# Kernel optimization log

Hardware: AMD Instinct MI355X
Metric: run time of the kernel (lower is better)

## Reference

```python
import jax, jax.numpy as jnp
import numpy as np

B, S, D = 4, 2048, 1024
KEY_DIM, VALUE_DIM = 1024, 1024
BETA = 1.0 / np.sqrt(D)  # beta defaults to 1/sqrt(input dim), per build()


def setup_inputs() -> dict:
    key = jax.random.key(0)
    ks = jax.random.split(key, 9)
    inv = 1.0 / np.sqrt(D)
    return {
        "query": jax.random.normal(ks[0], (B, S, D), dtype=jnp.float32),
        "key": jax.random.normal(ks[1], (B, S, D), dtype=jnp.float32),
        "value": jax.random.normal(ks[2], (B, S, D), dtype=jnp.float32),
        "Wq": jax.random.normal(ks[3], (D, KEY_DIM), dtype=jnp.float32) * inv,
        "bq": jnp.zeros((KEY_DIM,), dtype=jnp.float32),
        "Wk": jax.random.normal(ks[4], (D, KEY_DIM), dtype=jnp.float32) * inv,
        "bk": jnp.zeros((KEY_DIM,), dtype=jnp.float32),
        "Wv": jax.random.normal(ks[5], (D, VALUE_DIM), dtype=jnp.float32) * inv,
        "bv": jnp.zeros((VALUE_DIM,), dtype=jnp.float32),
    }


def reference(query, key, value, Wq, bq, Wk, bk, Wv, bv):
    # Dense projections
    q = query @ Wq + bq          # [B, S, key_dim]
    k = key @ Wk + bk            # [B, S, key_dim]
    v = value @ Wv + bv          # [B, S, value_dim]
    # Scaled dot-product attention (beta applied AFTER matmul, as in source)
    scores = jnp.einsum("bik,bjk->bij", q, k)  # [B, S, S]
    A = jax.nn.softmax(BETA * scores, axis=-1)
    return jnp.einsum("bij,bjk->bik", A, v)    # [B, S, value_dim]
```

## Files before the change

### kernel.cpp

```cpp
#include <hip/hip_runtime.h>


typedef __bf16 bf16x8 __attribute__((ext_vector_type(8)));
typedef float f32x4 __attribute__((ext_vector_type(4)));

#define MIB ((size_t)1 << 20)

__device__ __forceinline__ unsigned short f2b(float f) {
  unsigned int u = __float_as_uint(f);
  return (unsigned short)((u + 0x7FFFu + ((u >> 16) & 1u)) >> 16);
}

__device__ __forceinline__ void async16(const void* g, void* l) {
  __builtin_amdgcn_global_load_lds(
      (const __attribute__((address_space(1))) unsigned int*)g,
      (__attribute__((address_space(3))) unsigned int*)l, 16, 0, 0);
}

template <int TN>
__device__ __forceinline__ void gemm_loop(
    const unsigned short* __restrict__ A, const unsigned short* __restrict__ Bt,
    unsigned short* lds_a, unsigned short* lds_b, int K, int m0, int n0,
    f32x4 (&acc)[4][TN / 32]) {
  constexpr int NI = TN / 32;
  const int tid = threadIdx.x;
  const int lane = tid & 63;
  const int wave = tid >> 6;
  const int wm = (wave >> 1) * 64;
  const int wn = (wave & 1) * (TN / 2);
  const int fr = lane & 15;
  const int q = lane >> 4;

  for (int kb = 0; kb < K; kb += 64) {
#pragma unroll
    for (int i = 0; i < 4; ++i) {
      const int e = i * 256 + tid;
      const int r = e >> 3;
      const int cg = (e & 7) ^ (r & 7);
      async16(A + (size_t)(m0 + r) * K + kb + cg * 8, &lds_a[e * 8]);
    }
#pragma unroll
    for (int i = 0; i < TN / 32; ++i) {
      const int e = i * 256 + tid;
      const int r = e >> 3;
      const int cg = (e & 7) ^ (r & 7);
      async16(Bt + (size_t)(n0 + r) * K + kb + cg * 8, &lds_b[e * 8]);
    }
    __syncthreads();

#pragma unroll
    for (int ks = 0; ks < 64; ks += 32) {
      const int kc = (ks >> 3) + q;
      bf16x8 av[4], bv[NI];
#pragma unroll
      for (int mi = 0; mi < 4; ++mi) {
        const int R = wm + mi * 16 + fr;
        av[mi] = *(const bf16x8*)&lds_a[R * 64 + ((kc ^ (R & 7)) << 3)];
      }
#pragma unroll
      for (int ni = 0; ni < NI; ++ni) {
        const int R = wn + ni * 16 + fr;
        bv[ni] = *(const bf16x8*)&lds_b[R * 64 + ((kc ^ (R & 7)) << 3)];
      }
#pragma unroll
      for (int mi = 0; mi < 4; ++mi)
#pragma unroll
        for (int ni = 0; ni < NI; ++ni)
          acc[mi][ni] = __builtin_amdgcn_mfma_f32_16x16x32_bf16(
              av[mi], bv[ni], acc[mi][ni], 0, 0, 0);
    }
    __syncthreads();
  }
}

struct ProjArgs {
  const unsigned short* A[3];
  const unsigned short* Bt[3];
  unsigned short* C[3];
  const float* bias[3];
};

__global__ __launch_bounds__(256) void proj_gemm(ProjArgs p) {
  __shared__ __align__(16) unsigned short lds_a[128 * 64];
  __shared__ __align__(16) unsigned short lds_b[64 * 64];

  const int z = blockIdx.z;
  const int m0 = blockIdx.y * 128;
  const int n0 = blockIdx.x * 64;

  f32x4 acc[4][2] = {};
  gemm_loop<64>(p.A[z], p.Bt[z], lds_a, lds_b, 1024, m0, n0, acc);

  const int lane = threadIdx.x & 63;
  const int wave = threadIdx.x >> 6;
  const int wm = (wave >> 1) * 64;
  const int wn = (wave & 1) * 32;
  const int fr = lane & 15;
  const float* bias = p.bias[z];

  if (z != 2) {
    unsigned short* C = p.C[z];
#pragma unroll
    for (int mi = 0; mi < 4; ++mi) {
#pragma unroll
      for (int ni = 0; ni < 2; ++ni) {
        const int col = n0 + wn + ni * 16 + fr;
        const float bb = bias[col];
        const int rowb = m0 + wm + mi * 16 + (lane >> 4) * 4;
#pragma unroll
        for (int r = 0; r < 4; ++r)
          C[(size_t)(rowb + r) * 1024 + col] = f2b(acc[mi][ni][r] + bb);
      }
    }
  } else {
    unsigned short* C = p.C[2] + (size_t)(m0 >> 11) * (2048 * 1024);
#pragma unroll
    for (int mi = 0; mi < 4; ++mi) {
#pragma unroll
      for (int ni = 0; ni < 2; ++ni) {
        const int col = n0 + wn + ni * 16 + fr;
        const float bb = bias[col];
        const int rowb = (m0 + wm + mi * 16 + (lane >> 4) * 4) & 2047;
        ushort4 o = make_ushort4(f2b(acc[mi][ni][0] + bb), f2b(acc[mi][ni][1] + bb),
                                 f2b(acc[mi][ni][2] + bb), f2b(acc[mi][ni][3] + bb));
        *(ushort4*)&C[(size_t)col * 2048 + rowb] = o;
      }
    }
  }
}

template <int TN>
__global__ __launch_bounds__(256) void gemm_f32(
    const unsigned short* __restrict__ A, const unsigned short* __restrict__ Bt,
    float* __restrict__ C, int K, int ldc, long long sA, long long sB,
    long long sC) {
  __shared__ __align__(16) unsigned short lds_a[128 * 64];
  __shared__ __align__(16) unsigned short lds_b[TN * 64];
  const int bz = blockIdx.z;
  A += (long long)bz * sA;
  Bt += (long long)bz * sB;
  C += (long long)bz * sC;
  const int m0 = blockIdx.y * 128;
  const int n0 = blockIdx.x * TN;

  f32x4 acc[4][TN / 32] = {};
  gemm_loop<TN>(A, Bt, lds_a, lds_b, K, m0, n0, acc);

  const int lane = threadIdx.x & 63;
  const int wave = threadIdx.x >> 6;
  const int wm = (wave >> 1) * 64;
  const int wn = (wave & 1) * (TN / 2);
  const int fr = lane & 15;
#pragma unroll
  for (int mi = 0; mi < 4; ++mi) {
#pragma unroll
    for (int ni = 0; ni < TN / 32; ++ni) {
      const int col = n0 + wn + ni * 16 + fr;
      const int rowb = m0 + wm + mi * 16 + (lane >> 4) * 4;
#pragma unroll
      for (int r = 0; r < 4; ++r)
        C[(size_t)(rowb + r) * ldc + col] = acc[mi][ni][r];
    }
  }
}

__global__ __launch_bounds__(256) void cast3(
    const float4* __restrict__ a, const float4* __restrict__ b,
    const float4* __restrict__ c, ushort4* __restrict__ oa,
    ushort4* __restrict__ ob, ushort4* __restrict__ oc, int n4) {
  const int i = blockIdx.x * 256 + threadIdx.x;
  if (i >= n4) return;
  const float4* src = (blockIdx.y == 0) ? a : (blockIdx.y == 1) ? b : c;
  ushort4* dst = (blockIdx.y == 0) ? oa : (blockIdx.y == 1) ? ob : oc;
  float4 v = src[i];
  dst[i] = make_ushort4(f2b(v.x), f2b(v.y), f2b(v.z), f2b(v.w));
}

__global__ __launch_bounds__(256) void transpose3(
    const float* __restrict__ w0, const float* __restrict__ w1,
    const float* __restrict__ w2, unsigned short* __restrict__ t0,
    unsigned short* __restrict__ t1, unsigned short* __restrict__ t2) {
  __shared__ float t[32][33];
  const int K = 1024, N = 1024;
  const float* W = (blockIdx.z == 0) ? w0 : (blockIdx.z == 1) ? w1 : w2;
  unsigned short* WT = (blockIdx.z == 0) ? t0 : (blockIdx.z == 1) ? t1 : t2;
  const int n0 = blockIdx.x * 32, k0 = blockIdx.y * 32;
  const int tx = threadIdx.x, ty = threadIdx.y;
#pragma unroll
  for (int i = 0; i < 32; i += 8)
    t[ty + i][tx] = W[(size_t)(k0 + ty + i) * N + (n0 + tx)];
  __syncthreads();
#pragma unroll
  for (int i = 0; i < 32; i += 8)
    WT[(size_t)(n0 + ty + i) * K + (k0 + tx)] = f2b(t[tx][ty + i]);
}

__global__ __launch_bounds__(256) void softmax_rows(const float* __restrict__ S,
                                                    unsigned short* __restrict__ P) {
  const int cols = 2048;
  const size_t row = blockIdx.x;
  const float4* srow = (const float4*)(S + row * cols);
  const int tid = threadIdx.x;
  const int lane = tid & 63;
  const int wave = tid >> 6;

  float4 a = srow[tid];
  float4 b = srow[tid + 256];

  float mx = fmaxf(fmaxf(fmaxf(a.x, a.y), fmaxf(a.z, a.w)),
                   fmaxf(fmaxf(b.x, b.y), fmaxf(b.z, b.w)));
#pragma unroll
  for (int o = 1; o < 64; o <<= 1) mx = fmaxf(mx, __shfl_xor(mx, o));

  __shared__ float red[8];
  if (lane == 0) red[wave] = mx;
  __syncthreads();
  mx = fmaxf(fmaxf(red[0], red[1]), fmaxf(red[2], red[3]));

  const float c = 0.03125f * 1.4426950408889634f;
  float4 pa, pb;
  pa.x = exp2f((a.x - mx) * c); pa.y = exp2f((a.y - mx) * c);
  pa.z = exp2f((a.z - mx) * c); pa.w = exp2f((a.w - mx) * c);
  pb.x = exp2f((b.x - mx) * c); pb.y = exp2f((b.y - mx) * c);
  pb.z = exp2f((b.z - mx) * c); pb.w = exp2f((b.w - mx) * c);

  float sum = pa.x + pa.y + pa.z + pa.w + pb.x + pb.y + pb.z + pb.w;
#pragma unroll
  for (int o = 1; o < 64; o <<= 1) sum += __shfl_xor(sum, o);
  if (lane == 0) red[4 + wave] = sum;
  __syncthreads();
  sum = red[4] + red[5] + red[6] + red[7];

  const float inv = 1.0f / sum;
  ushort4* prow = (ushort4*)(P + row * cols);
  prow[tid] = make_ushort4(f2b(pa.x * inv), f2b(pa.y * inv), f2b(pa.z * inv),
                           f2b(pa.w * inv));
  prow[tid + 256] = make_ushort4(f2b(pb.x * inv), f2b(pb.y * inv),
                                 f2b(pb.z * inv), f2b(pb.w * inv));
}

extern "C" void kernel_launch(void* const* d_in, const int* in_sizes, int n_in,
                              void* d_out, int out_size, void* d_ws, size_t ws_size,
                              hipStream_t stream) {
  const float* query = (const float*)d_in[0];
  const float* key_ = (const float*)d_in[1];
  const float* value = (const float*)d_in[2];
  const float* Wq = (const float*)d_in[3];
  const float* bq = (const float*)d_in[4];
  const float* Wk = (const float*)d_in[5];
  const float* bk = (const float*)d_in[6];
  const float* Wv = (const float*)d_in[7];
  const float* bv = (const float*)d_in[8];
  float* out = (float*)d_out;

  char* ws = (char*)d_ws;
  unsigned short* WqT = (unsigned short*)ws;
  unsigned short* WkT = WqT + (size_t)1024 * 1024;
  unsigned short* WvT = WkT + (size_t)1024 * 1024;
  unsigned short* Xq = (unsigned short*)(ws + 6 * MIB);
  unsigned short* Xk = Xq + (size_t)8192 * 1024;
  unsigned short* Xv = Xk + (size_t)8192 * 1024;
  unsigned short* qb = (unsigned short*)(ws + 54 * MIB);
  unsigned short* kb = (unsigned short*)(ws + 70 * MIB);
  unsigned short* vT = (unsigned short*)(ws + 86 * MIB);
  float* sc = (float*)(ws + 102 * MIB);
  unsigned short* P = (unsigned short*)(ws + 6 * MIB);

  const int n4 = (4 * 2048 * 1024) / 4;
  cast3<<<dim3(n4 / 256, 3), 256, 0, stream>>>(
      (const float4*)query, (const float4*)key_, (const float4*)value,
      (ushort4*)Xq, (ushort4*)Xk, (ushort4*)Xv, n4);

  transpose3<<<dim3(32, 32, 3), dim3(32, 8), 0, stream>>>(Wq, Wk, Wv, WqT, WkT,
                                                          WvT);

  ProjArgs pa;
  pa.A[0] = Xq;  pa.A[1] = Xk;  pa.A[2] = Xv;
  pa.Bt[0] = WqT; pa.Bt[1] = WkT; pa.Bt[2] = WvT;
  pa.C[0] = qb;  pa.C[1] = kb;  pa.C[2] = vT;
  pa.bias[0] = bq; pa.bias[1] = bk; pa.bias[2] = bv;
  proj_gemm<<<dim3(16, 64, 3), 256, 0, stream>>>(pa);

  gemm_f32<64><<<dim3(32, 16, 4), 256, 0, stream>>>(
      qb, kb, sc, 1024, 2048, 2048LL * 1024, 2048LL * 1024, 2048LL * 2048);

  softmax_rows<<<8192, 256, 0, stream>>>(sc, P);

  gemm_f32<64><<<dim3(16, 16, 4), 256, 0, stream>>>(
      P, vT, out, 2048, 1024, 2048LL * 2048, 1024LL * 2048, 2048LL * 1024);
}
```

Before: 339.3 us.

## Replace GEMMs with 256x256 double-buffered 8-wave pipelined kernel and split-K PV

Replaces the 128x64 single-buffered GEMM loop with a 256x256 tile, 512-thread core that double-buffers LDS in half-tiles. It interleaves async global->LDS staging with MFMA quadrants, using raw barriers, explicit waitcnts and setprio. Projection and score GEMMs use this core. The PV GEMM is split in two along K for occupancy, writing two partial outputs that an extra add kernel sums. This raises data reuse and overlaps memory with compute, at the cost of 128KB LDS per block and an extra float buffer pass for the split-K reduction.

```diff
diff --git a/kernel.cpp b/kernel.cpp
--- a/kernel.cpp
+++ b/kernel.cpp
@@ -17,59 +17,164 @@
       (__attribute__((address_space(3))) unsigned int*)l, 16, 0, 0);
 }
 
-template <int TN>
-__device__ __forceinline__ void gemm_loop(
+__device__ __forceinline__ void barrier_raw() {
+  asm volatile("" ::: "memory");
+  __builtin_amdgcn_s_barrier();
+  asm volatile("" ::: "memory");
+}
+
+__device__ __forceinline__ void stage_half(
+    const unsigned short* __restrict__ src, unsigned short* dst, int ld,
+    int tid) {
+#pragma unroll
+  for (int i = 0; i < 2; ++i) {
+    const int e = i * 512 + tid;
+    const int r = e >> 3;
+    const int cg = (e & 7) ^ (r & 7);
+    async16(src + (size_t)r * ld + cg * 8, dst + e * 8);
+  }
+}
+
+template <int MO, int NO>
+__device__ __forceinline__ void quad16(f32x4 (&acc)[8][4],
+                                       const bf16x8 (&AV)[4][2],
+                                       const bf16x8 (&BV)[2][2]) {
+#pragma unroll
+  for (int mi = 0; mi < 4; ++mi)
+#pragma unroll
+    for (int ni = 0; ni < 2; ++ni)
+#pragma unroll
+      for (int ks = 0; ks < 2; ++ks)
+        acc[MO + mi][NO + ni] = __builtin_amdgcn_mfma_f32_16x16x32_bf16(
+            AV[mi][ks], BV[ni][ks], acc[MO + mi][NO + ni], 0, 0, 0);
+}
+
+__device__ __forceinline__ void gemm256_core(
     const unsigned short* __restrict__ A, const unsigned short* __restrict__ Bt,
-    unsigned short* lds_a, unsigned short* lds_b, int K, int m0, int n0,
-    f32x4 (&acc)[4][TN / 32]) {
-  constexpr int NI = TN / 32;
+    int K, int ld, int m0, int n0, unsigned short* lds, f32x4 (&acc)[8][4]) {
   const int tid = threadIdx.x;
   const int lane = tid & 63;
   const int wave = tid >> 6;
-  const int wm = (wave >> 1) * 64;
-  const int wn = (wave & 1) * (TN / 2);
+  const int wmh = wave >> 2;
+  const int wnh = (wave & 3) >> 1;
+  const int wno = (wave & 1) * 64;
   const int fr = lane & 15;
   const int q = lane >> 4;
-
-  for (int kb = 0; kb < K; kb += 64) {
-#pragma unroll
-    for (int i = 0; i < 4; ++i) {
-      const int e = i * 256 + tid;
-      const int r = e >> 3;
-      const int cg = (e & 7) ^ (r & 7);
-      async16(A + (size_t)(m0 + r) * K + kb + cg * 8, &lds_a[e * 8]);
-    }
-#pragma unroll
-    for (int i = 0; i < TN / 32; ++i) {
-      const int e = i * 256 + tid;
-      const int r = e >> 3;
-      const int cg = (e & 7) ^ (r & 7);
-      async16(Bt + (size_t)(n0 + r) * K + kb + cg * 8, &lds_b[e * 8]);
-    }
-    __syncthreads();
-
-#pragma unroll
-    for (int ks = 0; ks < 64; ks += 32) {
-      const int kc = (ks >> 3) + q;
-      bf16x8 av[4], bv[NI];
-#pragma unroll
-      for (int mi = 0; mi < 4; ++mi) {
-        const int R = wm + mi * 16 + fr;
-        av[mi] = *(const bf16x8*)&lds_a[R * 64 + ((kc ^ (R & 7)) << 3)];
+  const int NT = K >> 6;
+
+  auto ah = [&](int buf, int h) { return lds + buf * 32768 + h * 8192; };
+  auto bh = [&](int buf, int h) { return lds + buf * 32768 + 16384 + h * 8192; };
+
+  const unsigned short* gA[2] = {A + (size_t)m0 * ld,
+                                 A + (size_t)(m0 + 128) * ld};
+  const unsigned short* gB[2] = {Bt + (size_t)n0 * ld,
+                                 Bt + (size_t)(n0 + 128) * ld};
+
+  auto rdA = [&](bf16x8(&AV)[4][2], const unsigned short* aa, int ro) {
+#pragma unroll
+    for (int mi = 0; mi < 4; ++mi) {
+      const int r = ro + mi * 16 + fr;
+#pragma unroll
+      for (int ks = 0; ks < 2; ++ks) {
+        const int kc = (ks << 2) + q;
+        AV[mi][ks] = *(const bf16x8*)&aa[r * 64 + ((kc ^ (r & 7)) << 3)];
       }
-#pragma unroll
-      for (int ni = 0; ni < NI; ++ni) {
-        const int R = wn + ni * 16 + fr;
-        bv[ni] = *(const bf16x8*)&lds_b[R * 64 + ((kc ^ (R & 7)) << 3)];
+    }
+  };
+  auto rdB = [&](bf16x8(&BV)[2][2], const unsigned short* bb, int ro) {
+#pragma unroll
+    for (int ni = 0; ni < 2; ++ni) {
+      const int r = ro + ni * 16 + fr;
+#pragma unroll
+      for (int ks = 0; ks < 2; ++ks) {
+        const int kc = (ks << 2) + q;
+        BV[ni][ks] = *(const bf16x8*)&bb[r * 64 + ((kc ^ (r & 7)) << 3)];
       }
-#pragma unroll
-      for (int mi = 0; mi < 4; ++mi)
-#pragma unroll
-        for (int ni = 0; ni < NI; ++ni)
-          acc[mi][ni] = __builtin_amdgcn_mfma_f32_16x16x32_bf16(
-              av[mi], bv[ni], acc[mi][ni], 0, 0, 0);
-    }
-    __syncthreads();
+    }
+  };
+
+  stage_half(gB[0], bh(0, 0), ld, tid);
+  stage_half(gA[0], ah(0, 0), ld, tid);
+  stage_half(gB[1], bh(0, 1), ld, tid);
+  stage_half(gA[1], ah(0, 1), ld, tid);
+  stage_half(gB[0] + 64, bh(1, 0), ld, tid);
+  stage_half(gA[0] + 64, ah(1, 0), ld, tid);
+  asm volatile("s_waitcnt vmcnt(4)" ::: "memory");
+  barrier_raw();
+
+  for (int t = 0; t < NT; ++t) {
+    const int buf = t & 1;
+    const unsigned short* a = ah(buf, wmh);
+    const unsigned short* b = bh(buf, wnh);
+    bf16x8 av[4][2], bv0[2][2], bv1[2][2];
+
+    rdA(av, a, 0);
+    rdB(bv0, b, wno);
+    if (t + 1 < NT)
+      stage_half(gB[1] + (size_t)(t + 1) * 64, bh((t + 1) & 1, 1), ld, tid);
+    asm volatile("s_waitcnt lgkmcnt(8)" ::: "memory");
+    barrier_raw();
+    asm volatile("s_waitcnt lgkmcnt(0)" ::: "memory");
+    __builtin_amdgcn_s_setprio(1);
+    quad16<0, 0>(acc, av, bv0);
+    __builtin_amdgcn_s_setprio(0);
+    barrier_raw();
+
+    rdB(bv1, b, wno + 32);
+    if (t + 1 < NT)
+      stage_half(gA[1] + (size_t)(t + 1) * 64, ah((t + 1) & 1, 1), ld, tid);
+    barrier_raw();
+    asm volatile("s_waitcnt lgkmcnt(0)" ::: "memory");
+    __builtin_amdgcn_s_setprio(1);
+    quad16<0, 2>(acc, av, bv1);
+    __builtin_amdgcn_s_setprio(0);
+    barrier_raw();
+
+    rdA(av, a, 64);
+    if (t + 2 < NT)
+      stage_half(gB[0] + (size_t)(t + 2) * 64, bh(buf, 0), ld, tid);
+    barrier_raw();
+    asm volatile("s_waitcnt lgkmcnt(0)" ::: "memory");
+    __builtin_amdgcn_s_setprio(1);
+    quad16<4, 2>(acc, av, bv1);
+    __builtin_amdgcn_s_setprio(0);
+    barrier_raw();
+
+    if (t + 2 < NT)
+      stage_half(gA[0] + (size_t)(t + 2) * 64, ah(buf, 0), ld, tid);
+    barrier_raw();
+    __builtin_amdgcn_s_setprio(1);
+    quad16<4, 0>(acc, av, bv0);
+    __builtin_amdgcn_s_setprio(0);
+    if (t + 2 < NT) {
+      asm volatile("s_waitcnt vmcnt(4)" ::: "memory");
+    } else if (t + 1 < NT) {
+      asm volatile("s_waitcnt vmcnt(0)" ::: "memory");
+    }
+    barrier_raw();
+  }
+}
+
+__device__ __forceinline__ void store_f32(float* __restrict__ C, int ldc,
+                                          int m0, int n0,
+                                          const f32x4 (&acc)[8][4]) {
+  const int tid = threadIdx.x;
+  const int lane = tid & 63;
+  const int wave = tid >> 6;
+  const int wm = (wave >> 2) * 128;
+  const int wn = (wave & 3) * 64;
+  const int fr = lane & 15;
+  const int q4 = (lane >> 4) * 4;
+#pragma unroll
+  for (int mi = 0; mi < 8; ++mi) {
+    const int rowb = m0 + wm + mi * 16 + q4;
+#pragma unroll
+    for (int ni = 0; ni < 4; ++ni) {
+      const int col = n0 + wn + ni * 16 + fr;
+#pragma unroll
+      for (int r = 0; r < 4; ++r)
+        C[(size_t)(rowb + r) * ldc + col] = acc[mi][ni][r];
+    }
   }
 }
 
@@ -80,33 +185,33 @@
   const float* bias[3];
 };
 
-__global__ __launch_bounds__(256) void proj_gemm(ProjArgs p) {
-  __shared__ __align__(16) unsigned short lds_a[128 * 64];
-  __shared__ __align__(16) unsigned short lds_b[64 * 64];
-
+__global__ __launch_bounds__(512, 2) void proj_gemm8(ProjArgs p) {
+  __shared__ __align__(16) unsigned short lds[65536];
   const int z = blockIdx.z;
-  const int m0 = blockIdx.y * 128;
-  const int n0 = blockIdx.x * 64;
-
-  f32x4 acc[4][2] = {};
-  gemm_loop<64>(p.A[z], p.Bt[z], lds_a, lds_b, 1024, m0, n0, acc);
-
-  const int lane = threadIdx.x & 63;
-  const int wave = threadIdx.x >> 6;
-  const int wm = (wave >> 1) * 64;
-  const int wn = (wave & 1) * 32;
+  const int m0 = blockIdx.y * 256;
+  const int n0 = blockIdx.x * 256;
+
+  f32x4 acc[8][4] = {};
+  gemm256_core(p.A[z], p.Bt[z], 1024, 1024, m0, n0, lds, acc);
+
+  const int tid = threadIdx.x;
+  const int lane = tid & 63;
+  const int wave = tid >> 6;
+  const int wm = (wave >> 2) * 128;
+  const int wn = (wave & 3) * 64;
   const int fr = lane & 15;
+  const int q4 = (lane >> 4) * 4;
   const float* bias = p.bias[z];
 
   if (z != 2) {
     unsigned short* C = p.C[z];
 #pragma unroll
-    for (int mi = 0; mi < 4; ++mi) {
-#pragma unroll
-      for (int ni = 0; ni < 2; ++ni) {
-        const int col = n0 + wn + ni * 16 + fr;
-        const float bb = bias[col];
-        const int rowb = m0 + wm + mi * 16 + (lane >> 4) * 4;
+    for (int ni = 0; ni < 4; ++ni) {
+      const int col = n0 + wn + ni * 16 + fr;
+      const float bb = bias[col];
+#pragma unroll
+      for (int mi = 0; mi < 8; ++mi) {
+        const int rowb = m0 + wm + mi * 16 + q4;
 #pragma unroll
         for (int r = 0; r < 4; ++r)
           C[(size_t)(rowb + r) * 1024 + col] = f2b(acc[mi][ni][r] + bb);
@@ -114,54 +219,60 @@
     }
   } else {
     unsigned short* C = p.C[2] + (size_t)(m0 >> 11) * (2048 * 1024);
-#pragma unroll
-    for (int mi = 0; mi < 4; ++mi) {
-#pragma unroll
-      for (int ni = 0; ni < 2; ++ni) {
-        const int col = n0 + wn + ni * 16 + fr;
-        const float bb = bias[col];
-        const int rowb = (m0 + wm + mi * 16 + (lane >> 4) * 4) & 2047;
-        ushort4 o = make_ushort4(f2b(acc[mi][ni][0] + bb), f2b(acc[mi][ni][1] + bb),
-                                 f2b(acc[mi][ni][2] + bb), f2b(acc[mi][ni][3] + bb));
+    const int rloc = (m0 & 2047) + wm;
+#pragma unroll
+    for (int ni = 0; ni < 4; ++ni) {
+      const int col = n0 + wn + ni * 16 + fr;
+      const float bb = bias[col];
+#pragma unroll
+      for (int mi = 0; mi < 8; ++mi) {
+        const int rowb = rloc + mi * 16 + q4;
+        ushort4 o =
+            make_ushort4(f2b(acc[mi][ni][0] + bb), f2b(acc[mi][ni][1] + bb),
+                         f2b(acc[mi][ni][2] + bb), f2b(acc[mi][ni][3] + bb));
         *(ushort4*)&C[(size_t)col * 2048 + rowb] = o;
       }
     }
   }
 }
 
-template <int TN>
-__global__ __launch_bounds__(256) void gemm_f32(
-    const unsigned short* __restrict__ A, const unsigned short* __restrict__ Bt,
-    float* __restrict__ C, int K, int ldc, long long sA, long long sB,
-    long long sC) {
-  __shared__ __align__(16) unsigned short lds_a[128 * 64];
-  __shared__ __align__(16) unsigned short lds_b[TN * 64];
+__global__ __launch_bounds__(512, 2) void score_gemm8(
+    const unsigned short* __restrict__ qb, const unsigned short* __restrict__ kb,
+    float* __restrict__ sc) {
+  __shared__ __align__(16) unsigned short lds[65536];
   const int bz = blockIdx.z;
-  A += (long long)bz * sA;
-  Bt += (long long)bz * sB;
-  C += (long long)bz * sC;
-  const int m0 = blockIdx.y * 128;
-  const int n0 = blockIdx.x * TN;
-
-  f32x4 acc[4][TN / 32] = {};
-  gemm_loop<TN>(A, Bt, lds_a, lds_b, K, m0, n0, acc);
-
-  const int lane = threadIdx.x & 63;
-  const int wave = threadIdx.x >> 6;
-  const int wm = (wave >> 1) * 64;
-  const int wn = (wave & 1) * (TN / 2);
-  const int fr = lane & 15;
-#pragma unroll
-  for (int mi = 0; mi < 4; ++mi) {
-#pragma unroll
-    for (int ni = 0; ni < TN / 32; ++ni) {
-      const int col = n0 + wn + ni * 16 + fr;
-      const int rowb = m0 + wm + mi * 16 + (lane >> 4) * 4;
-#pragma unroll
-      for (int r = 0; r < 4; ++r)
-        C[(size_t)(rowb + r) * ldc + col] = acc[mi][ni][r];
-    }
-  }
+  const int m0 = blockIdx.y * 256;
+  const int n0 = blockIdx.x * 256;
+  f32x4 acc[8][4] = {};
+  gemm256_core(qb + (size_t)bz * (2048 * 1024), kb + (size_t)bz * (2048 * 1024),
+               1024, 1024, m0, n0, lds, acc);
+  store_f32(sc + (size_t)bz * (2048 * 2048), 2048, m0, n0, acc);
+}
+
+__global__ __launch_bounds__(512, 2) void pv_gemm8(
+    const unsigned short* __restrict__ P, const unsigned short* __restrict__ vT,
+    float* __restrict__ parts) {
+  __shared__ __align__(16) unsigned short lds[65536];
+  const int bz = blockIdx.z >> 1;
+  const int kh = blockIdx.z & 1;
+  const int m0 = blockIdx.y * 256;
+  const int n0 = blockIdx.x * 256;
+  f32x4 acc[8][4] = {};
+  gemm256_core(P + (size_t)bz * (2048 * 2048) + (size_t)kh * 1024,
+               vT + (size_t)bz * (1024 * 2048) + (size_t)kh * 1024, 1024, 2048,
+               m0, n0, lds, acc);
+  store_f32(parts + (size_t)kh * (4 * 2048 * 1024) +
+                (size_t)bz * (2048 * 1024),
+            1024, m0, n0, acc);
+}
+
+__global__ __launch_bounds__(256) void add2(const float4* __restrict__ a,
+                                            const float4* __restrict__ b,
+                                            float4* __restrict__ o, int n4) {
+  const int i = blockIdx.x * 256 + threadIdx.x;
+  if (i >= n4) return;
+  float4 x = a[i], y = b[i];
+  o[i] = make_float4(x.x + y.x, x.y + y.y, x.z + y.z, x.w + y.w);
 }
 
 __global__ __launch_bounds__(256) void cast3(
@@ -265,6 +376,8 @@
   unsigned short* vT = (unsigned short*)(ws + 86 * MIB);
   float* sc = (float*)(ws + 102 * MIB);
   unsigned short* P = (unsigned short*)(ws + 6 * MIB);
+  float* part0 = sc;
+  float* part1 = sc + (size_t)4 * 2048 * 1024;
 
   const int n4 = (4 * 2048 * 1024) / 4;
   cast3<<<dim3(n4 / 256, 3), 256, 0, stream>>>(
@@ -279,13 +392,14 @@
   pa.Bt[0] = WqT; pa.Bt[1] = WkT; pa.Bt[2] = WvT;
   pa.C[0] = qb;  pa.C[1] = kb;  pa.C[2] = vT;
   pa.bias[0] = bq; pa.bias[1] = bk; pa.bias[2] = bv;
-  proj_gemm<<<dim3(16, 64, 3), 256, 0, stream>>>(pa);
-
-  gemm_f32<64><<<dim3(32, 16, 4), 256, 0, stream>>>(
-      qb, kb, sc, 1024, 2048, 2048LL * 1024, 2048LL * 1024, 2048LL * 2048);
+  proj_gemm8<<<dim3(4, 32, 3), 512, 0, stream>>>(pa);
+
+  score_gemm8<<<dim3(8, 8, 4), 512, 0, stream>>>(qb, kb, sc);
 
   softmax_rows<<<8192, 256, 0, stream>>>(sc, P);
 
-  gemm_f32<64><<<dim3(16, 16, 4), 256, 0, stream>>>(
-      P, vT, out, 2048, 1024, 2048LL * 2048, 1024LL * 2048, 2048LL * 1024);
-}
+  pv_gemm8<<<dim3(4, 8, 8), 512, 0, stream>>>(P, vT, part0);
+
+  add2<<<dim3(n4 / 256), 256, 0, stream>>>(
+      (const float4*)part0, (const float4*)part1, (float4*)out, n4);
+}
```

Measured after the change: 338.4 us. No clear change (-0.3%).
